# Kernel optimization log

Hardware: AMD Instinct MI355X
Metric: run time of the kernel (lower is better)

The kernel has to match this reference:

```python
import jax, jax.numpy as jnp
import numpy as np

N_MOTIF_PER_CLASS = 8
N_CLASS = 16
N_MOTIF = N_MOTIF_PER_CLASS * N_CLASS
TEMPERATURE = 0.2
TAU = 0.99
K2 = 32
EPS = 1e-4


def setup_inputs() -> dict:
    key = jax.random.key(0)
    k1, k2, k3 = jax.random.split(key, 3)
    N, H = 32768, 1024
    z = jax.random.normal(k1, (N, H), dtype=jnp.float32)
    Motif_Vector = jax.random.normal(k2, (N_MOTIF, H), dtype=jnp.float32)
    y = jax.random.randint(k3, (N,), 0, N_CLASS, dtype=jnp.int64)
    return {"z": z, "Motif_Vector": Motif_Vector, "y": y}


def euclidean_1(X, M):
    # squared euclidean distance via GEMM, then log-ratio similarity
    xp = X @ M.T                                     # [N, n_motif]
    distance = (-2.0 * xp
                + jnp.sum(X * X, axis=1, keepdims=True)
                + jnp.sum(M * M, axis=1)[None, :])
    similarity = jnp.log((distance + 1.0) / (distance + EPS))
    return similarity, distance


def reference(z, Motif_Vector, y):
    similarity, distance = euclidean_1(z, Motif_Vector)

    # mapping: motif j belongs to class j // n_motif_per_class
    motif_class = jnp.arange(N_MOTIF) // N_MOTIF_PER_CLASS   # [n_motif]
    true_motifs = (y[:, None] == motif_class[None, :])       # [N, n_motif]

    # contrastive loss (exact torch math: exp(sim/T), max over positives,
    # sum over negatives)
    sims = jnp.exp(similarity / TEMPERATURE)
    sim_pos = jnp.max(jnp.where(true_motifs, sims, -jnp.inf), axis=1)
    sim_neg_sum = jnp.sum(jnp.where(true_motifs, 0.0, sims), axis=1)
    loss = -jnp.mean(jnp.log(sim_pos / (sim_neg_sum + sim_pos)))

    # update_motif (update_type='topk', weighted_mean=False):
    # torch passes `distance` into filter_similar_graph and argsorts
    # descending, i.e. selects the K2 LARGEST distances among same-class
    # samples (faithful to source).
    masked = jnp.where(true_motifs.T, distance.T, -jnp.inf)  # [n_motif, N]
    _, idx = jax.lax.top_k(masked, K2)                       # [n_motif, K2]
    selected = z[idx]                                        # [n_motif, K2, H]
    new_motif = jnp.mean(selected, axis=1)                   # weights = 1/K2
    new_M = TAU * Motif_Vector + (1.0 - TAU) * new_motif

    return loss, new_M
```

## Files before the change

kernel.cpp:

```cpp
#include <hip/hip_runtime.h>
#include <cstdint>
#include <cmath>

#define NROWS 32768
#define HD    1024
#define NMOT  128
#define NCLS  16
#define KSEL  32
#define EPSV  1e-4f

typedef __attribute__((ext_vector_type(4))) float  f32x4;
typedef __attribute__((ext_vector_type(8))) __bf16 bf16x8;
typedef __attribute__((ext_vector_type(4))) __bf16 bf16x4;
typedef unsigned long long u64;

#define WS_LP   0
#define WS_MN   512
#define WS_MVBF 1024
#define WS_S1K  66560
#define WS_CD   197632
#define CAPC    256

static __device__ __forceinline__ float dot4(float4 v) {
    return v.x * v.x + v.y * v.y + v.z * v.z + v.w * v.w;
}

static __device__ __forceinline__ bf16x4 cvt4(float4 v) {
    bf16x4 t;
    t[0] = (__bf16)v.x; t[1] = (__bf16)v.y; t[2] = (__bf16)v.z; t[3] = (__bf16)v.w;
    return t;
}

static __device__ __forceinline__ bf16x8 cvt8(float4 a, float4 b) {
    bf16x8 t;
    t[0] = (__bf16)a.x; t[1] = (__bf16)a.y; t[2] = (__bf16)a.z; t[3] = (__bf16)a.w;
    t[4] = (__bf16)b.x; t[5] = (__bf16)b.y; t[6] = (__bf16)b.z; t[7] = (__bf16)b.w;
    return t;
}

static __device__ __forceinline__ u64 pack_key(float v, int idx) {
    unsigned int b = __float_as_uint(v);
    unsigned int mo = (b & 0x80000000u) ? ~b : (b | 0x80000000u);
    unsigned int khi = ~mo;
    return ((u64)khi << 32) | (unsigned int)idx;
}

__global__ __launch_bounds__(256) void prep_k(const float* __restrict__ mv,
                                              float* __restrict__ mn,
                                              __bf16* __restrict__ mvbf) {
    const int b = blockIdx.x;
    const int tid = threadIdx.x;
    const int k = tid * 4;
    float4 v = *(const float4*)&mv[(size_t)b * HD + k];
    *(bf16x4*)&mvbf[(size_t)b * HD + k] = cvt4(v);
    float s = dot4(v);
#pragma unroll
    for (int o = 1; o < 64; o <<= 1) s += __shfl_xor(s, o, 64);
    __shared__ float red[4];
    if ((tid & 63) == 0) red[tid >> 6] = s;
    __syncthreads();
    if (tid == 0) mn[b] = red[0] + red[1] + red[2] + red[3];
}

#define BM 64
#define BK 32
#define NS (HD / BK)

__global__ __launch_bounds__(256, 2) void gemm_fused(
    const float* __restrict__ z, const __bf16* __restrict__ mvbf,
    const float* __restrict__ mn, float* __restrict__ cd,
    const int* __restrict__ y, float* __restrict__ lossP) {
    __shared__ float redw[4];

    const int tid  = threadIdx.x;
    const int lane = tid & 63;
    const int wid  = tid >> 6;
    const int l15  = lane & 15;
    const int quad = lane >> 4;
    const int row0 = blockIdx.x * BM;
    const int myrow = row0 + wid * 16 + l15;

    const float* zrow = z + (size_t)myrow * HD + quad * 8;

    const __bf16* bbase[8];
#pragma unroll
    for (int j = 0; j < 8; ++j)
        bbase[j] = mvbf + (size_t)(j * 16 + l15) * HD + quad * 8;

    float mcv[8];
#pragma unroll
    for (int j = 0; j < 8; ++j) mcv[j] = mn[j * 16 + l15];
    const int yv = y[myrow];

    f32x4 acc[8];
#pragma unroll
    for (int j = 0; j < 8; ++j) acc[j] = (f32x4){0.f, 0.f, 0.f, 0.f};
    float zsq = 0.f;

    bf16x8 rb[2][8];
    float4 ra[2][2];
#pragma unroll
    for (int j = 0; j < 8; ++j) rb[0][j] = *(const bf16x8*)(bbase[j]);
    ra[0][0] = *(const float4*)(zrow);
    ra[0][1] = *(const float4*)(zrow + 4);
    ra[1][0] = *(const float4*)(zrow + BK);
    ra[1][1] = *(const float4*)(zrow + BK + 4);

#pragma unroll
    for (int kt = 0; kt < NS; ++kt) {
        const int s = kt & 1;
        bf16x8 af = cvt8(ra[s][0], ra[s][1]);
        zsq += dot4(ra[s][0]) + dot4(ra[s][1]);
        if (kt + 2 < NS) {
            ra[s][0] = *(const float4*)(zrow + (kt + 2) * BK);
            ra[s][1] = *(const float4*)(zrow + (kt + 2) * BK + 4);
        }
        if (kt + 1 < NS) {
#pragma unroll
            for (int j = 0; j < 8; ++j)
                rb[s ^ 1][j] = *(const bf16x8*)(bbase[j] + (kt + 1) * BK);
        }
#pragma unroll
        for (int j = 0; j < 8; ++j)
            acc[j] = __builtin_amdgcn_mfma_f32_16x16x32_bf16(
                af, rb[s][j], acc[j], 0, 0, 0);
    }

    zsq += __shfl_xor(zsq, 16, 64);
    zsq += __shfl_xor(zsq, 32, 64);

    float znv[4]; int rcls[4];
#pragma unroll
    for (int reg = 0; reg < 4; ++reg) {
        znv[reg]  = __shfl(zsq, quad * 4 + reg, 64);
        rcls[reg] = __shfl(yv,  quad * 4 + reg, 64);
    }
    float pm[4], ns[4];
#pragma unroll
    for (int reg = 0; reg < 4; ++reg) { pm[reg] = 0.f; ns[reg] = 0.f; }

#pragma unroll
    for (int j = 0; j < 8; ++j) {
        const int c = j * 16 + l15;
        const float mc = mcv[j];
        const int ccls = c >> 3;
#pragma unroll
        for (int reg = 0; reg < 4; ++reg) {
            float d = znv[reg] + mc - 2.f * acc[j][reg];
            float r = (d + 1.0f) * __builtin_amdgcn_rcpf(d + EPSV);
            float r2 = r * r;
            float s = r2 * r2 * r;
            if (ccls == rcls[reg]) {
                pm[reg] = fmaxf(pm[reg], s);
                const int row = row0 + wid * 16 + quad * 4 + reg;
                cd[(size_t)row * 8 + (c & 7)] = d;
            } else {
                ns[reg] += s;
            }
        }
    }
#pragma unroll
    for (int o = 1; o < 16; o <<= 1)
#pragma unroll
        for (int reg = 0; reg < 4; ++reg) {
            pm[reg] = fmaxf(pm[reg], __shfl_xor(pm[reg], o, 64));
            ns[reg] += __shfl_xor(ns[reg], o, 64);
        }
    float li = 0.f;
    if (l15 == 0) {
#pragma unroll
        for (int reg = 0; reg < 4; ++reg)
            li += logf((ns[reg] + pm[reg]) / pm[reg]);
    }
    li += __shfl_xor(li, 16, 64);
    li += __shfl_xor(li, 32, 64);
    if (lane == 0) redw[wid] = li;
    __syncthreads();
    if (tid == 0) lossP[blockIdx.x] = redw[0] + redw[1] + redw[2] + redw[3];
}

__global__ __launch_bounds__(256) void sel1_k(const int* __restrict__ y,
                                              const float* __restrict__ cd,
                                              u64* __restrict__ s1k) {
    __shared__ u64 keys[256];
    __shared__ int clist[CAPC];
    __shared__ int cnt;

    const int bid = blockIdx.x;
    const int j = bid >> 4, chunk = bid & 15;
    const int cls = j >> 3, m8 = j & 7;
    const int tid = threadIdx.x;
    const int lane = tid & 63;

    if (tid == 0) cnt = 0;
    __syncthreads();
    const int base = chunk * 2048;
#pragma unroll
    for (int t = 0; t < 8; ++t) {
        const int i = base + t * 256 + tid;
        const bool pred = (y[i] == cls);
        const u64 m = __ballot(pred);
        int wbase = 0;
        if (lane == 0 && m) wbase = atomicAdd(&cnt, (int)__popcll(m));
        wbase = __shfl(wbase, 0, 64);
        if (pred) {
            const int p = wbase + (int)__popcll(m & ((1ull << lane) - 1ull));
            if (p < CAPC) clist[p] = i;
        }
    }
    __syncthreads();
    const int n = cnt < CAPC ? cnt : CAPC;

    u64 key = ~0ull;
    if (tid < n) {
        const int idx = clist[tid];
        key = pack_key(cd[(size_t)idx * 8 + m8], idx);
    }
    keys[tid] = key;
    __syncthreads();

    for (int k = 2; k <= 256; k <<= 1) {
        for (int jj = k >> 1; jj > 0; jj >>= 1) {
            if (tid < 128) {
                const int i  = ((tid & ~(jj - 1)) << 1) | (tid & (jj - 1));
                const int ix = i | jj;
                const u64 A = keys[i], B = keys[ix];
                const bool up = ((i & k) == 0);
                if ((A > B) == up) { keys[i] = B; keys[ix] = A; }
            }
            __syncthreads();
        }
    }
    if (tid < KSEL) s1k[(size_t)j * 512 + chunk * KSEL + tid] = keys[tid];
}

__global__ __launch_bounds__(256) void merge_k(
    const float* __restrict__ z, const float* __restrict__ mv,
    const u64* __restrict__ s1k, const float* __restrict__ lossP,
    float* __restrict__ out) {
    __shared__ u64 keys[512];
    __shared__ int sel[KSEL];
    __shared__ float redf[4];

    const int b = blockIdx.x;
    const int j = b >> 2, q = b & 3;
    const int tid = threadIdx.x;
    const int lane = tid & 63;
    const int wave = tid >> 6;

    if (b == 0) {
        float s = lossP[tid] + lossP[tid + 256];
#pragma unroll
        for (int o = 1; o < 64; o <<= 1) s += __shfl_xor(s, o, 64);
        if (lane == 0) redf[wave] = s;
        __syncthreads();
        if (tid == 0)
            out[0] = (redf[0] + redf[1] + redf[2] + redf[3]) * (1.0f / NROWS);
    }

    keys[tid]       = s1k[(size_t)j * 512 + tid];
    keys[tid + 256] = s1k[(size_t)j * 512 + 256 + tid];
    __syncthreads();

    for (int k = 2; k <= 512; k <<= 1) {
        for (int jj = k >> 1; jj > 0; jj >>= 1) {
            const int i  = ((tid & ~(jj - 1)) << 1) | (tid & (jj - 1));
            const int ix = i | jj;
            const u64 A = keys[i], B = keys[ix];
            const bool up = ((i & k) == 0);
            if ((A > B) == up) { keys[i] = B; keys[ix] = A; }
            __syncthreads();
        }
    }
    if (tid < KSEL) sel[tid] = (int)(keys[tid] & 0xFFFFFFFFu);
    __syncthreads();

    const int h = q * 256 + tid;
    float s = 0.f;
#pragma unroll 8
    for (int r = 0; r < KSEL; ++r) s += z[(size_t)sel[r] * HD + h];
    out[1 + (size_t)j * HD + h] =
        0.99f * mv[(size_t)j * HD + h] + 0.01f * (s * (1.0f / KSEL));
}

extern "C" void kernel_launch(void* const* d_in, const int* in_sizes, int n_in,
                              void* d_out, int out_size, void* d_ws, size_t ws_size,
                              hipStream_t stream) {
    const float* z  = (const float*)d_in[0];
    const float* mv = (const float*)d_in[1];
    const int*   y  = (const int*)d_in[2];
    float* out = (float*)d_out;
    float* wsf = (float*)d_ws;
    float*  lossP = wsf + WS_LP;
    float*  mn    = wsf + WS_MN;
    __bf16* mvbf  = (__bf16*)(wsf + WS_MVBF);
    u64*    s1k   = (u64*)(wsf + WS_S1K);
    float*  cd    = wsf + WS_CD;

    hipLaunchKernelGGL(prep_k,     dim3(NMOT),       dim3(256), 0, stream,
                       mv, mn, mvbf);
    hipLaunchKernelGGL(gemm_fused, dim3(NROWS / BM), dim3(256), 0, stream,
                       z, mvbf, mn, cd, y, lossP);
    hipLaunchKernelGGL(sel1_k,     dim3(NMOT * 16),  dim3(256), 0, stream,
                       y, cd, s1k);
    hipLaunchKernelGGL(merge_k,    dim3(NMOT * 4),   dim3(256), 0, stream,
                       z, mv, s1k, lossP, out);
}
```

Measured before the change: 263.3 us.

## Stage motif tile in LDS, split motifs across blocks, deepen z prefetch

The GEMM kernel now runs 256 blocks of 512 threads. Each block copies half of the bf16 motif matrix (64 motifs × 1024) into LDS via global_load_lds, then sweeps 256 rows in two passes, instead of every wave re-reading B from global memory. z is prefetched four stages deep with inline-asm loads and explicit vmcnt waits. Because each block now covers only half the motifs, per-row negative sums and positive maxima go to workspace, and the loss log-reduction moves into sel1_k. The price is z being read twice (once per motif half), a 128KB LDS footprint limiting occupancy to one block per CU, and fragile hand-written waitcnt scheduling.

```diff
diff --git a/kernel.cpp b/kernel.cpp
--- a/kernel.cpp
+++ b/kernel.cpp
@@ -19,10 +19,15 @@
 #define WS_MVBF 1024
 #define WS_S1K  66560
 #define WS_CD   197632
+#define WS_PNS  459776
+#define WS_PM   525312
 #define CAPC    256
 
 static __device__ __forceinline__ float dot4(float4 v) {
     return v.x * v.x + v.y * v.y + v.z * v.z + v.w * v.w;
+}
+static __device__ __forceinline__ float dot4v(f32x4 v) {
+    return v[0] * v[0] + v[1] * v[1] + v[2] * v[2] + v[3] * v[3];
 }
 
 static __device__ __forceinline__ bf16x4 cvt4(float4 v) {
@@ -31,12 +36,27 @@
     return t;
 }
 
-static __device__ __forceinline__ bf16x8 cvt8(float4 a, float4 b) {
+static __device__ __forceinline__ bf16x8 cvt8v(f32x4 a, f32x4 b) {
     bf16x8 t;
-    t[0] = (__bf16)a.x; t[1] = (__bf16)a.y; t[2] = (__bf16)a.z; t[3] = (__bf16)a.w;
-    t[4] = (__bf16)b.x; t[5] = (__bf16)b.y; t[6] = (__bf16)b.z; t[7] = (__bf16)b.w;
+    t[0] = (__bf16)a[0]; t[1] = (__bf16)a[1]; t[2] = (__bf16)a[2]; t[3] = (__bf16)a[3];
+    t[4] = (__bf16)b[0]; t[5] = (__bf16)b[1]; t[6] = (__bf16)b[2]; t[7] = (__bf16)b[3];
     return t;
 }
+
+static __device__ __forceinline__ void gl16(const void* g, void* l) {
+    __builtin_amdgcn_global_load_lds(
+        (const __attribute__((address_space(1))) void*)g,
+        (__attribute__((address_space(3))) void*)l, 16, 0, 0);
+}
+
+#define LOADA(dst, base, imm)                                        \
+    asm volatile("global_load_dwordx4 %0, %1, off offset:%2"         \
+                 : "=&v"(dst) : "v"(base), "n"(imm))
+
+#define WAITV6 asm volatile("s_waitcnt vmcnt(6)" ::: "memory")
+#define WAITV4 asm volatile("s_waitcnt vmcnt(4)" ::: "memory")
+#define WAITV2 asm volatile("s_waitcnt vmcnt(2)" ::: "memory")
+#define WAITV0 asm volatile("s_waitcnt vmcnt(0)" ::: "memory")
 
 static __device__ __forceinline__ u64 pack_key(float v, int idx) {
     unsigned int b = __float_as_uint(v);
@@ -62,129 +82,150 @@
     if (tid == 0) mn[b] = red[0] + red[1] + red[2] + red[3];
 }
 
-#define BM 64
 #define BK 32
 #define NS (HD / BK)
 
-__global__ __launch_bounds__(256, 2) void gemm_fused(
+__global__ __launch_bounds__(512, 1) void gemm_fused(
     const float* __restrict__ z, const __bf16* __restrict__ mvbf,
     const float* __restrict__ mn, float* __restrict__ cd,
-    const int* __restrict__ y, float* __restrict__ lossP) {
-    __shared__ float redw[4];
+    const int* __restrict__ y, float* __restrict__ pns,
+    float* __restrict__ pmr) {
+    __shared__ __align__(16) __bf16 Bs[65536];
 
     const int tid  = threadIdx.x;
     const int lane = tid & 63;
     const int wid  = tid >> 6;
     const int l15  = lane & 15;
     const int quad = lane >> 4;
-    const int row0 = blockIdx.x * BM;
-    const int myrow = row0 + wid * 16 + l15;
-
-    const float* zrow = z + (size_t)myrow * HD + quad * 8;
-
-    const __bf16* bbase[8];
-#pragma unroll
-    for (int j = 0; j < 8; ++j)
-        bbase[j] = mvbf + (size_t)(j * 16 + l15) * HD + quad * 8;
-
-    float mcv[8];
-#pragma unroll
-    for (int j = 0; j < 8; ++j) mcv[j] = mn[j * 16 + l15];
-    const int yv = y[myrow];
-
-    f32x4 acc[8];
-#pragma unroll
-    for (int j = 0; j < 8; ++j) acc[j] = (f32x4){0.f, 0.f, 0.f, 0.f};
-    float zsq = 0.f;
-
-    bf16x8 rb[2][8];
-    float4 ra[2][2];
-#pragma unroll
-    for (int j = 0; j < 8; ++j) rb[0][j] = *(const bf16x8*)(bbase[j]);
-    ra[0][0] = *(const float4*)(zrow);
-    ra[0][1] = *(const float4*)(zrow + 4);
-    ra[1][0] = *(const float4*)(zrow + BK);
-    ra[1][1] = *(const float4*)(zrow + BK + 4);
-
-#pragma unroll
-    for (int kt = 0; kt < NS; ++kt) {
-        const int s = kt & 1;
-        bf16x8 af = cvt8(ra[s][0], ra[s][1]);
-        zsq += dot4(ra[s][0]) + dot4(ra[s][1]);
-        if (kt + 2 < NS) {
-            ra[s][0] = *(const float4*)(zrow + (kt + 2) * BK);
-            ra[s][1] = *(const float4*)(zrow + (kt + 2) * BK + 4);
-        }
-        if (kt + 1 < NS) {
-#pragma unroll
-            for (int j = 0; j < 8; ++j)
-                rb[s ^ 1][j] = *(const bf16x8*)(bbase[j] + (kt + 1) * BK);
-        }
-#pragma unroll
-        for (int j = 0; j < 8; ++j)
-            acc[j] = __builtin_amdgcn_mfma_f32_16x16x32_bf16(
-                af, rb[s][j], acc[j], 0, 0, 0);
-    }
-
-    zsq += __shfl_xor(zsq, 16, 64);
-    zsq += __shfl_xor(zsq, 32, 64);
-
-    float znv[4]; int rcls[4];
-#pragma unroll
-    for (int reg = 0; reg < 4; ++reg) {
-        znv[reg]  = __shfl(zsq, quad * 4 + reg, 64);
-        rcls[reg] = __shfl(yv,  quad * 4 + reg, 64);
-    }
-    float pm[4], ns[4];
-#pragma unroll
-    for (int reg = 0; reg < 4; ++reg) { pm[reg] = 0.f; ns[reg] = 0.f; }
-
-#pragma unroll
-    for (int j = 0; j < 8; ++j) {
-        const int c = j * 16 + l15;
-        const float mc = mcv[j];
-        const int ccls = c >> 3;
+    const int h    = blockIdx.x & 1;
+    const int rg   = blockIdx.x >> 1;
+
+    char* bsb = (char*)Bs;
+
+#pragma unroll
+    for (int i = 0; i < 16; ++i) {
+        const int c  = wid * 16 + i;
+        const int kt = c >> 2, j = c & 3;
+        const __bf16* src =
+            mvbf + (size_t)(h * 64 + j * 16 + l15) * HD + kt * 32 + quad * 8;
+        gl16(src, bsb + c * 1024);
+    }
+    __syncthreads();
+
+    for (int p = 0; p < 2; ++p) {
+        const int rowp  = rg * 256 + p * 128;
+        const int myrow = rowp + wid * 16 + l15;
+        const float* zb = z + (size_t)myrow * HD + quad * 8;
+
+        f32x4 acc[4];
+#pragma unroll
+        for (int j = 0; j < 4; ++j) acc[j] = (f32x4){0.f, 0.f, 0.f, 0.f};
+        float zsq = 0.f;
+
+        f32x4  ra[4][2];
+        bf16x8 bfr[2][4];
+
+#pragma unroll
+        for (int s = 0; s < 4; ++s) {
+            LOADA(ra[s][0], zb, s * 128);
+            LOADA(ra[s][1], zb, s * 128 + 16);
+        }
+#pragma unroll
+        for (int j = 0; j < 4; ++j)
+            bfr[0][j] = *(const bf16x8*)(bsb + j * 1024 + lane * 16);
+
+#pragma unroll
+        for (int kt = 0; kt < NS; ++kt) {
+            if (kt + 4 <= NS)      WAITV6;
+            else if (kt == NS - 3) WAITV4;
+            else if (kt == NS - 2) WAITV2;
+            else                   WAITV0;
+            __builtin_amdgcn_sched_barrier(0);
+
+            const int sl = kt & 3, cb = kt & 1;
+            zsq += dot4v(ra[sl][0]) + dot4v(ra[sl][1]);
+            bf16x8 af = cvt8v(ra[sl][0], ra[sl][1]);
+            if (kt + 4 < NS) {
+                LOADA(ra[sl][0], zb, (kt + 4) * 128);
+                LOADA(ra[sl][1], zb, (kt + 4) * 128 + 16);
+            }
+            if (kt + 1 < NS) {
+#pragma unroll
+                for (int j = 0; j < 4; ++j)
+                    bfr[cb ^ 1][j] = *(const bf16x8*)(
+                        bsb + ((kt + 1) * 4 + j) * 1024 + lane * 16);
+            }
+#pragma unroll
+            for (int j = 0; j < 4; ++j)
+                acc[j] = __builtin_amdgcn_mfma_f32_16x16x32_bf16(
+                    af, bfr[cb][j], acc[j], 0, 0, 0);
+        }
+
+        zsq += __shfl_xor(zsq, 16, 64);
+        zsq += __shfl_xor(zsq, 32, 64);
+        const int yv = y[myrow];
+        float mcv[4];
+#pragma unroll
+        for (int j = 0; j < 4; ++j) mcv[j] = mn[h * 64 + j * 16 + l15];
+
+        float znv[4]; int rcls[4];
 #pragma unroll
         for (int reg = 0; reg < 4; ++reg) {
-            float d = znv[reg] + mc - 2.f * acc[j][reg];
-            float r = (d + 1.0f) * __builtin_amdgcn_rcpf(d + EPSV);
-            float r2 = r * r;
-            float s = r2 * r2 * r;
-            if (ccls == rcls[reg]) {
-                pm[reg] = fmaxf(pm[reg], s);
-                const int row = row0 + wid * 16 + quad * 4 + reg;
-                cd[(size_t)row * 8 + (c & 7)] = d;
-            } else {
-                ns[reg] += s;
-            }
-        }
-    }
-#pragma unroll
-    for (int o = 1; o < 16; o <<= 1)
-#pragma unroll
-        for (int reg = 0; reg < 4; ++reg) {
-            pm[reg] = fmaxf(pm[reg], __shfl_xor(pm[reg], o, 64));
-            ns[reg] += __shfl_xor(ns[reg], o, 64);
-        }
-    float li = 0.f;
-    if (l15 == 0) {
-#pragma unroll
-        for (int reg = 0; reg < 4; ++reg)
-            li += logf((ns[reg] + pm[reg]) / pm[reg]);
-    }
-    li += __shfl_xor(li, 16, 64);
-    li += __shfl_xor(li, 32, 64);
-    if (lane == 0) redw[wid] = li;
-    __syncthreads();
-    if (tid == 0) lossP[blockIdx.x] = redw[0] + redw[1] + redw[2] + redw[3];
+            znv[reg]  = __shfl(zsq, quad * 4 + reg, 64);
+            rcls[reg] = __shfl(yv,  quad * 4 + reg, 64);
+        }
+        float pm[4], ns[4];
+#pragma unroll
+        for (int reg = 0; reg < 4; ++reg) { pm[reg] = 0.f; ns[reg] = 0.f; }
+
+#pragma unroll
+        for (int j = 0; j < 4; ++j) {
+            const int c = h * 64 + j * 16 + l15;
+            const float mc = mcv[j];
+            const int ccls = c >> 3;
+#pragma unroll
+            for (int reg = 0; reg < 4; ++reg) {
+                float d = znv[reg] + mc - 2.f * acc[j][reg];
+                float r = (d + 1.0f) * __builtin_amdgcn_rcpf(d + EPSV);
+                float r2 = r * r;
+                float s = r2 * r2 * r;
+                if (ccls == rcls[reg]) {
+                    pm[reg] = fmaxf(pm[reg], s);
+                    const int row = rowp + wid * 16 + quad * 4 + reg;
+                    cd[(size_t)row * 8 + (c & 7)] = d;
+                } else {
+                    ns[reg] += s;
+                }
+            }
+        }
+#pragma unroll
+        for (int o = 1; o < 16; o <<= 1)
+#pragma unroll
+            for (int reg = 0; reg < 4; ++reg) {
+                pm[reg] = fmaxf(pm[reg], __shfl_xor(pm[reg], o, 64));
+                ns[reg] += __shfl_xor(ns[reg], o, 64);
+            }
+        if (l15 == 0) {
+#pragma unroll
+            for (int reg = 0; reg < 4; ++reg) {
+                const int row = rowp + wid * 16 + quad * 4 + reg;
+                pns[row * 2 + h] = ns[reg];
+                if ((rcls[reg] >> 3) == h) pmr[row] = pm[reg];
+            }
+        }
+    }
 }
 
 __global__ __launch_bounds__(256) void sel1_k(const int* __restrict__ y,
                                               const float* __restrict__ cd,
-                                              u64* __restrict__ s1k) {
+                                              u64* __restrict__ s1k,
+                                              const float* __restrict__ pns,
+                                              const float* __restrict__ pmr,
+                                              float* __restrict__ lossP) {
     __shared__ u64 keys[256];
     __shared__ int clist[CAPC];
     __shared__ int cnt;
+    __shared__ float lred[4];
 
     const int bid = blockIdx.x;
     const int j = bid >> 4, chunk = bid & 15;
@@ -232,6 +273,22 @@
         }
     }
     if (tid < KSEL) s1k[(size_t)j * 512 + chunk * KSEL + tid] = keys[tid];
+
+    if (j == 0) {
+        float li = 0.f;
+#pragma unroll
+        for (int t = 0; t < 8; ++t) {
+            const int row = base + t * 256 + tid;
+            const float pm = pmr[row];
+            const float nst = pns[row * 2] + pns[row * 2 + 1];
+            li += logf((nst + pm) / pm);
+        }
+#pragma unroll
+        for (int o = 1; o < 64; o <<= 1) li += __shfl_xor(li, o, 64);
+        if (lane == 0) lred[tid >> 6] = li;
+        __syncthreads();
+        if (tid == 0) lossP[chunk] = lred[0] + lred[1] + lred[2] + lred[3];
+    }
 }
 
 __global__ __launch_bounds__(256) void merge_k(
@@ -240,22 +297,16 @@
     float* __restrict__ out) {
     __shared__ u64 keys[512];
     __shared__ int sel[KSEL];
-    __shared__ float redf[4];
 
     const int b = blockIdx.x;
     const int j = b >> 2, q = b & 3;
     const int tid = threadIdx.x;
-    const int lane = tid & 63;
-    const int wave = tid >> 6;
-
-    if (b == 0) {
-        float s = lossP[tid] + lossP[tid + 256];
-#pragma unroll
-        for (int o = 1; o < 64; o <<= 1) s += __shfl_xor(s, o, 64);
-        if (lane == 0) redf[wave] = s;
-        __syncthreads();
-        if (tid == 0)
-            out[0] = (redf[0] + redf[1] + redf[2] + redf[3]) * (1.0f / NROWS);
+
+    if (b == 0 && tid < 64) {
+        float li = (tid < 16) ? lossP[tid] : 0.f;
+#pragma unroll
+        for (int o = 1; o < 64; o <<= 1) li += __shfl_xor(li, o, 64);
+        if (tid == 0) out[0] = li * (1.0f / NROWS);
     }
 
     keys[tid]       = s1k[(size_t)j * 512 + tid];
@@ -296,13 +347,15 @@
     __bf16* mvbf  = (__bf16*)(wsf + WS_MVBF);
     u64*    s1k   = (u64*)(wsf + WS_S1K);
     float*  cd    = wsf + WS_CD;
-
-    hipLaunchKernelGGL(prep_k,     dim3(NMOT),       dim3(256), 0, stream,
+    float*  pns   = wsf + WS_PNS;
+    float*  pmr   = wsf + WS_PM;
+
+    hipLaunchKernelGGL(prep_k,     dim3(NMOT),      dim3(256), 0, stream,
                        mv, mn, mvbf);
-    hipLaunchKernelGGL(gemm_fused, dim3(NROWS / BM), dim3(256), 0, stream,
-                       z, mvbf, mn, cd, y, lossP);
-    hipLaunchKernelGGL(sel1_k,     dim3(NMOT * 16),  dim3(256), 0, stream,
-                       y, cd, s1k);
-    hipLaunchKernelGGL(merge_k,    dim3(NMOT * 4),   dim3(256), 0, stream,
+    hipLaunchKernelGGL(gemm_fused, dim3(256),       dim3(512), 0, stream,
+                       z, mvbf, mn, cd, y, pns, pmr);
+    hipLaunchKernelGGL(sel1_k,     dim3(NMOT * 16), dim3(256), 0, stream,
+                       y, cd, s1k, pns, pmr, lossP);
+    hipLaunchKernelGGL(merge_k,    dim3(NMOT * 4),  dim3(256), 0, stream,
                        z, mv, s1k, lossP, out);
 }
```

Measured after the change: 229.4 us. -12.9%, faster.

## Stage motif bf16 tiles in LDS via async global_load_lds with deeper A prefetch

Applied to the files above, without the earlier changes.

The GEMM kernel now uses 512-thread blocks covering 128 rows, and 256 blocks, one per CU. The bf16 motif matrix is double-buffered into 128KB of LDS in chunks of 256 columns using global_load_lds, rather than each wave reading B directly from global/L2. The z rows are prefetched four steps ahead with inline-asm loads and manual vmcnt waits. This removes redundant per-wave B traffic from L2 and deepens latency hiding. The cost is fragile hand-tuned waitcnt logic and one block per CU. The loss reduction is adjusted to the new count of 256 partials.

```diff
diff --git a/kernel.cpp b/kernel.cpp
--- a/kernel.cpp
+++ b/kernel.cpp
@@ -24,6 +24,9 @@
 static __device__ __forceinline__ float dot4(float4 v) {
     return v.x * v.x + v.y * v.y + v.z * v.z + v.w * v.w;
 }
+static __device__ __forceinline__ float dot4v(f32x4 v) {
+    return v[0] * v[0] + v[1] * v[1] + v[2] * v[2] + v[3] * v[3];
+}
 
 static __device__ __forceinline__ bf16x4 cvt4(float4 v) {
     bf16x4 t;
@@ -31,12 +34,24 @@
     return t;
 }
 
-static __device__ __forceinline__ bf16x8 cvt8(float4 a, float4 b) {
+static __device__ __forceinline__ bf16x8 cvt8v(f32x4 a, f32x4 b) {
     bf16x8 t;
-    t[0] = (__bf16)a.x; t[1] = (__bf16)a.y; t[2] = (__bf16)a.z; t[3] = (__bf16)a.w;
-    t[4] = (__bf16)b.x; t[5] = (__bf16)b.y; t[6] = (__bf16)b.z; t[7] = (__bf16)b.w;
+    t[0] = (__bf16)a[0]; t[1] = (__bf16)a[1]; t[2] = (__bf16)a[2]; t[3] = (__bf16)a[3];
+    t[4] = (__bf16)b[0]; t[5] = (__bf16)b[1]; t[6] = (__bf16)b[2]; t[7] = (__bf16)b[3];
     return t;
 }
+
+static __device__ __forceinline__ void gl16(const void* g, void* l) {
+    __builtin_amdgcn_global_load_lds(
+        (const __attribute__((address_space(1))) void*)g,
+        (__attribute__((address_space(3))) void*)l, 16, 0, 0);
+}
+
+#define LOADA(dst, base, imm)                                        \
+    asm volatile("global_load_dwordx4 %0, %1, off offset:%2"         \
+                 : "=&v"(dst) : "v"(base), "n"(imm))
+
+#define WAITN(n) asm volatile("s_waitcnt vmcnt(" #n ")" ::: "memory")
 
 static __device__ __forceinline__ u64 pack_key(float v, int idx) {
     unsigned int b = __float_as_uint(v);
@@ -62,72 +77,106 @@
     if (tid == 0) mn[b] = red[0] + red[1] + red[2] + red[3];
 }
 
-#define BM 64
 #define BK 32
-#define NS (HD / BK)
-
-__global__ __launch_bounds__(256, 2) void gemm_fused(
+#define NS 32
+#define SPC 8
+
+__global__ __launch_bounds__(512, 1) void gemm_fused(
     const float* __restrict__ z, const __bf16* __restrict__ mvbf,
     const float* __restrict__ mn, float* __restrict__ cd,
     const int* __restrict__ y, float* __restrict__ lossP) {
-    __shared__ float redw[4];
+    __shared__ __align__(16) __bf16 Bs[2][32768];
+    __shared__ float redw[8];
 
     const int tid  = threadIdx.x;
     const int lane = tid & 63;
     const int wid  = tid >> 6;
     const int l15  = lane & 15;
     const int quad = lane >> 4;
-    const int row0 = blockIdx.x * BM;
-    const int myrow = row0 + wid * 16 + l15;
-
-    const float* zrow = z + (size_t)myrow * HD + quad * 8;
-
-    const __bf16* bbase[8];
-#pragma unroll
-    for (int j = 0; j < 8; ++j)
-        bbase[j] = mvbf + (size_t)(j * 16 + l15) * HD + quad * 8;
-
-    float mcv[8];
-#pragma unroll
-    for (int j = 0; j < 8; ++j) mcv[j] = mn[j * 16 + l15];
-    const int yv = y[myrow];
+    const int rg   = blockIdx.x;
+    const int myrow = rg * 128 + wid * 16 + l15;
+
+    const float* zb = z + (size_t)myrow * HD + quad * 8;
+
+    char* bs0 = (char*)Bs[0];
+    char* bs1 = (char*)Bs[1];
+
+#pragma unroll
+    for (int i = 0; i < 8; ++i)
+        gl16(mvbf + (size_t)(i * 16 + l15) * HD + wid * 32 + quad * 8,
+             bs0 + (wid * 8 + i) * 1024);
+
+    f32x4 ra[4][2];
+#pragma unroll
+    for (int s = 0; s < 4; ++s) {
+        LOADA(ra[s][0], zb, s * 128);
+        LOADA(ra[s][1], zb, s * 128 + 16);
+    }
+    WAITN(6);
+    __builtin_amdgcn_sched_barrier(0);
+    __builtin_amdgcn_s_barrier();
+    asm volatile("" ::: "memory");
 
     f32x4 acc[8];
 #pragma unroll
     for (int j = 0; j < 8; ++j) acc[j] = (f32x4){0.f, 0.f, 0.f, 0.f};
     float zsq = 0.f;
 
-    bf16x8 rb[2][8];
-    float4 ra[2][2];
-#pragma unroll
-    for (int j = 0; j < 8; ++j) rb[0][j] = *(const bf16x8*)(bbase[j]);
-    ra[0][0] = *(const float4*)(zrow);
-    ra[0][1] = *(const float4*)(zrow + 4);
-    ra[1][0] = *(const float4*)(zrow + BK);
-    ra[1][1] = *(const float4*)(zrow + BK + 4);
-
-#pragma unroll
-    for (int kt = 0; kt < NS; ++kt) {
-        const int s = kt & 1;
-        bf16x8 af = cvt8(ra[s][0], ra[s][1]);
-        zsq += dot4(ra[s][0]) + dot4(ra[s][1]);
-        if (kt + 2 < NS) {
-            ra[s][0] = *(const float4*)(zrow + (kt + 2) * BK);
-            ra[s][1] = *(const float4*)(zrow + (kt + 2) * BK + 4);
-        }
-        if (kt + 1 < NS) {
+#pragma unroll
+    for (int kc = 0; kc < 4; ++kc) {
+        const char* bsc = ((kc & 1) ? bs1 : bs0) + lane * 16;
+        if (kc + 1 < 4) {
+            char* bsn = (((kc + 1) & 1) ? bs1 : bs0);
+#pragma unroll
+            for (int i = 0; i < 8; ++i)
+                gl16(mvbf + (size_t)(i * 16 + l15) * HD + (kc + 1) * 256 +
+                         wid * 32 + quad * 8,
+                     bsn + (wid * 8 + i) * 1024);
+        }
+#pragma unroll
+        for (int m = 0; m < SPC; ++m) {
+            const int kt = kc * SPC + m;
+            if (kc < 3) {
+                if (m < 4) WAITN(14); else WAITN(6);
+            } else {
+                if (m <= 4) WAITN(6);
+                else if (m == 5) WAITN(4);
+                else if (m == 6) WAITN(2);
+                else WAITN(0);
+            }
+            __builtin_amdgcn_sched_barrier(0);
+
+            bf16x8 bfr[8];
 #pragma unroll
             for (int j = 0; j < 8; ++j)
-                rb[s ^ 1][j] = *(const bf16x8*)(bbase[j] + (kt + 1) * BK);
-        }
-#pragma unroll
-        for (int j = 0; j < 8; ++j)
-            acc[j] = __builtin_amdgcn_mfma_f32_16x16x32_bf16(
-                af, rb[s][j], acc[j], 0, 0, 0);
+                bfr[j] = *(const bf16x8*)(bsc + (m * 8 + j) * 1024);
+
+            const int sl = kt & 3;
+            zsq += dot4v(ra[sl][0]) + dot4v(ra[sl][1]);
+            bf16x8 af = cvt8v(ra[sl][0], ra[sl][1]);
+            if (kt + 4 < NS) {
+                LOADA(ra[sl][0], zb, (kt + 4) * 128);
+                LOADA(ra[sl][1], zb, (kt + 4) * 128 + 16);
+            }
+#pragma unroll
+            for (int j = 0; j < 8; ++j)
+                acc[j] = __builtin_amdgcn_mfma_f32_16x16x32_bf16(
+                    af, bfr[j], acc[j], 0, 0, 0);
+        }
+        if (kc < 3) {
+            asm volatile("s_waitcnt lgkmcnt(0)" ::: "memory");
+            __builtin_amdgcn_s_barrier();
+            asm volatile("" ::: "memory");
+            __builtin_amdgcn_sched_barrier(0);
+        }
     }
 
     zsq += __shfl_xor(zsq, 16, 64);
     zsq += __shfl_xor(zsq, 32, 64);
+    const int yv = y[myrow];
+    float mcv[8];
+#pragma unroll
+    for (int j = 0; j < 8; ++j) mcv[j] = mn[j * 16 + l15];
 
     float znv[4]; int rcls[4];
 #pragma unroll
@@ -152,7 +201,7 @@
             float s = r2 * r2 * r;
             if (ccls == rcls[reg]) {
                 pm[reg] = fmaxf(pm[reg], s);
-                const int row = row0 + wid * 16 + quad * 4 + reg;
+                const int row = rg * 128 + wid * 16 + quad * 4 + reg;
                 cd[(size_t)row * 8 + (c & 7)] = d;
             } else {
                 ns[reg] += s;
@@ -176,7 +225,12 @@
     li += __shfl_xor(li, 32, 64);
     if (lane == 0) redw[wid] = li;
     __syncthreads();
-    if (tid == 0) lossP[blockIdx.x] = redw[0] + redw[1] + redw[2] + redw[3];
+    if (tid == 0) {
+        float t = 0.f;
+#pragma unroll
+        for (int w = 0; w < 8; ++w) t += redw[w];
+        lossP[blockIdx.x] = t;
+    }
 }
 
 __global__ __launch_bounds__(256) void sel1_k(const int* __restrict__ y,
@@ -249,7 +303,7 @@
     const int wave = tid >> 6;
 
     if (b == 0) {
-        float s = lossP[tid] + lossP[tid + 256];
+        float s = lossP[tid];
 #pragma unroll
         for (int o = 1; o < 64; o <<= 1) s += __shfl_xor(s, o, 64);
         if (lane == 0) redf[wave] = s;
@@ -297,12 +351,12 @@
     u64*    s1k   = (u64*)(wsf + WS_S1K);
     float*  cd    = wsf + WS_CD;
 
-    hipLaunchKernelGGL(prep_k,     dim3(NMOT),       dim3(256), 0, stream,
+    hipLaunchKernelGGL(prep_k,     dim3(NMOT),      dim3(256), 0, stream,
                        mv, mn, mvbf);
-    hipLaunchKernelGGL(gemm_fused, dim3(NROWS / BM), dim3(256), 0, stream,
+    hipLaunchKernelGGL(gemm_fused, dim3(256),       dim3(512), 0, stream,
                        z, mvbf, mn, cd, y, lossP);
-    hipLaunchKernelGGL(sel1_k,     dim3(NMOT * 16),  dim3(256), 0, stream,
+    hipLaunchKernelGGL(sel1_k,     dim3(NMOT * 16), dim3(256), 0, stream,
                        y, cd, s1k);
-    hipLaunchKernelGGL(merge_k,    dim3(NMOT * 4),   dim3(256), 0, stream,
+    hipLaunchKernelGGL(merge_k,    dim3(NMOT * 4),  dim3(256), 0, stream,
                        z, mv, s1k, lossP, out);
 }
```

After: 233.0 us. 11.5% less time.
